# Performance work log

Hardware: AMD Instinct MI355X
Metric: run time of the kernel (lower is better)

The kernel has to match this reference:

```python
import jax, jax.numpy as jnp
import numpy as np

DEGREE = 3
N_BASIS = 16


def _clamped_knots(n_basis, degree):
    # Clamped uniform knot vector on [0, 1]: degree+1 repeated knots at each end.
    n_interior = n_basis - degree - 1
    interior = np.linspace(0.0, 1.0, n_interior + 2)[1:-1]
    knots = np.concatenate([np.zeros(degree + 1), interior, np.ones(degree + 1)])
    return jnp.asarray(knots, dtype=jnp.float32)


def bspline_basis(x, degree=DEGREE, n_basis=N_BASIS):
    # Cox-de Boor recursion, vectorized over all leading dims of x.
    # x: (...,) in [0,1] -> (..., n_basis)
    t = _clamped_knots(n_basis, degree)
    n_knots = n_basis + degree + 1
    xe = jnp.clip(x, 0.0, 1.0 - 1e-6)[..., None]
    B = ((xe >= t[:-1]) & (xe < t[1:])).astype(x.dtype)  # (..., n_knots-1)
    for p in range(1, degree + 1):
        dl = t[p:n_knots - 1] - t[:n_knots - 1 - p]
        dr = t[p + 1:n_knots] - t[1:n_knots - p]
        left = jnp.where(dl > 0, (xe - t[:n_knots - 1 - p]) / jnp.where(dl > 0, dl, 1.0), 0.0)
        right = jnp.where(dr > 0, (t[p + 1:n_knots] - xe) / jnp.where(dr > 0, dr, 1.0), 0.0)
        B = left * B[..., :-1] + right * B[..., 1:]
    return B  # (..., n_basis)


def _kl(cm, lv):
    # KL(N(cm, exp(lv)) || N(0, 1)) summed over all edges/coeffs (prior_scale = 1).
    var = jnp.exp(lv)
    return 0.5 * jnp.sum(var + cm * cm - 1.0 - lv)


def _layer(x, cm, lv):
    # x: (B, in); cm, lv: (out, in, n_basis)
    basis = bspline_basis(x)  # (B, in, n_basis)
    out = jnp.einsum('bik,oik->bo', basis, cm)  # fused per-edge weighted sum
    return out, _kl(cm, lv)


def setup_inputs() -> dict:
    key = jax.random.key(0)
    ks = jax.random.split(key, 4)
    B = 8192
    sizes = [256, 512, 512, 256]
    nb = N_BASIS
    inp = {"x": jax.random.uniform(ks[0], (B, sizes[0]), dtype=jnp.float32)}
    for i in range(3):
        inp[f"cm{i}"] = 0.1 * jax.random.normal(ks[1 + i], (sizes[i + 1], sizes[i], nb), dtype=jnp.float32)
        inp[f"lv{i}"] = -2.0 * jnp.ones((sizes[i + 1], sizes[i], nb), dtype=jnp.float32)
    return inp


def reference(x, cm0, lv0, cm1, lv1, cm2, lv2):
    out = x
    kl = jnp.zeros((), x.dtype)
    for cm, lv in ((cm0, lv0), (cm1, lv1), (cm2, lv2)):
        out, k = _layer(out, cm, lv)
        kl = kl + k
    return out, kl
```

## Files before the change

### kernel.cpp

```cpp
#include <hip/hip_runtime.h>
#include <hip/hip_bf16.h>


typedef __attribute__((ext_vector_type(8))) _Float16 f16x8;
typedef __attribute__((ext_vector_type(4))) float float4v;
typedef unsigned short ushort_t;

__device__ __forceinline__ ushort_t f2h(float f) {
  _Float16 h = (_Float16)f;
  return *(ushort_t*)&h;
}
__device__ __forceinline__ float h2f(ushort_t u) {
  return (float)*(_Float16*)&u;
}

__device__ __forceinline__ void bspline_w4(float x, int& k0, float w[4]) {
  const float XMAX = 1.0f - 1e-6f;
  float xe = fminf(fmaxf(x, 0.0f), XMAX);
  int cell = (int)(xe * 13.0f);
  cell = cell > 12 ? 12 : cell;
  k0 = cell;
  int j = cell + 3;
  const float s = 1.0f / 13.0f;
  int cjm2 = max(j - 5, 0);
  int cjm1 = max(j - 4, 0);
  int cj   = j - 3;
  int cj1  = j - 2;
  int cj2  = min(j - 1, 13);
  int cj3  = min(j, 13);
  float tjm1 = cjm1 * s, tj = cj * s;
  float tjm2 = cjm2 * s;
  float tj1 = cj1 * s, tj2 = cj2 * s, tj3 = cj3 * s;
  float left1 = xe - tj, left2 = xe - tjm1, left3 = xe - tjm2;
  float right1 = tj1 - xe, right2 = tj2 - xe, right3 = tj3 - xe;
#define INV3(d) ((d) == 1 ? 13.0f : ((d) == 2 ? 6.5f : (13.0f / 3.0f)))
  float i10 = INV3(cj1 - cj);
  float i20 = INV3(cj1 - cjm1), i21 = INV3(cj2 - cj);
  float i30 = INV3(cj1 - cjm2), i31 = INV3(cj2 - cjm1), i32 = INV3(cj3 - cj);
#undef INV3
  float temp = i10;
  float N0 = right1 * temp;
  float N1 = left1 * temp;
  temp = N0 * i20;
  N0 = right1 * temp;
  float saved = left2 * temp;
  temp = N1 * i21;
  N1 = saved + right2 * temp;
  float N2 = left1 * temp;
  temp = N0 * i30;
  N0 = right1 * temp;
  saved = left3 * temp;
  temp = N1 * i31;
  N1 = saved + right2 * temp;
  saved = left2 * temp;
  temp = N2 * i32;
  N2 = saved + right3 * temp;
  float N3 = left1 * temp;
  w[0] = N0; w[1] = N1; w[2] = N2; w[3] = N3;
}

template <bool SPLIT_A>
__global__ __launch_bounds__(256, 2) void kan_layer(
    const float* __restrict__ act, const ushort_t* __restrict__ Bsw,
    float* __restrict__ outp, int IN, int OUT) {
  const int K = IN * 16;
  const int KC = K >> 3;
  __shared__ ushort_t Ah[128 * 72];
  __shared__ ushort_t Al[SPLIT_A ? 128 * 72 : 1];

  const int tid = threadIdx.x;
  const int lane = tid & 63;
  const int wv = tid >> 6;
  const int wm = wv >> 1, wn = wv & 1;
  const int quad = lane >> 4, l15 = lane & 15;
  const int b0 = blockIdx.x * 128;
  const int n0 = blockIdx.y * 128;
  const int tbase = (n0 >> 4) + wn * 4;

  float4v acc[4][4];
#pragma unroll
  for (int a = 0; a < 4; a++)
#pragma unroll
    for (int b = 0; b < 4; b++) acc[a][b] = (float4v)0.0f;

  const int gm = tid >> 1;
  const int gip = (tid & 1) * 2;

  const int nsteps = K / 64;
  const int chunk = nsteps / gridDim.z;
  const int kbeg = blockIdx.z * chunk;
  const int kend = kbeg + chunk;
  for (int kstep = kbeg; kstep < kend; ++kstep) {
    const int i0 = kstep * 4;

    const float2 xv = *(const float2*)&act[(size_t)(b0 + gm) * IN + i0 + gip];
    f16x8 bfrag[2][4];
#pragma unroll
    for (int ks = 0; ks < 2; ++ks)
#pragma unroll
      for (int nt = 0; nt < 4; ++nt) {
        size_t eoff = (((size_t)(tbase + nt)) * KC + kstep * 8 + ks * 4) * 128
                      + lane * 8;
        bfrag[ks][nt] = *(const f16x8*)&Bsw[eoff];
      }

    int k0a, k0b; float wa[4], wb[4];
    bspline_w4(xv.x, k0a, wa);
    bspline_w4(xv.y, k0b, wb);

    __syncthreads();

    {
      uint4 z; z.x = z.y = z.z = z.w = 0u;
      ushort_t* arow_h = &Ah[gm * 72 + gip * 16];
      ((uint4*)arow_h)[0] = z; ((uint4*)arow_h)[1] = z;
      ((uint4*)arow_h)[2] = z; ((uint4*)arow_h)[3] = z;
#pragma unroll
      for (int t = 0; t < 4; ++t) {
        arow_h[k0a + t] = f2h(wa[t]);
        arow_h[16 + k0b + t] = f2h(wb[t]);
      }
      if (SPLIT_A) {
        ushort_t* arow_l = &Al[gm * 72 + gip * 16];
        ((uint4*)arow_l)[0] = z; ((uint4*)arow_l)[1] = z;
        ((uint4*)arow_l)[2] = z; ((uint4*)arow_l)[3] = z;
#pragma unroll
        for (int t = 0; t < 4; ++t) {
          arow_l[k0a + t] = f2h(wa[t] - h2f(f2h(wa[t])));
          arow_l[16 + k0b + t] = f2h(wb[t] - h2f(f2h(wb[t])));
        }
      }
    }
    __syncthreads();

#pragma unroll
    for (int ks = 0; ks < 2; ++ks) {
      f16x8 ah[4], al[4];
#pragma unroll
      for (int mt = 0; mt < 4; ++mt) {
        int off = (wm * 64 + mt * 16 + l15) * 72 + ks * 32 + quad * 8;
        ah[mt] = *(const f16x8*)&Ah[off];
        if (SPLIT_A) al[mt] = *(const f16x8*)&Al[off];
      }
#pragma unroll
      for (int mt = 0; mt < 4; ++mt)
#pragma unroll
        for (int nt = 0; nt < 4; ++nt) {
          if (SPLIT_A)
            acc[mt][nt] = __builtin_amdgcn_mfma_f32_16x16x32_f16(al[mt], bfrag[ks][nt], acc[mt][nt], 0, 0, 0);
          acc[mt][nt] = __builtin_amdgcn_mfma_f32_16x16x32_f16(ah[mt], bfrag[ks][nt], acc[mt][nt], 0, 0, 0);
        }
    }
  }

#pragma unroll
  for (int mt = 0; mt < 4; ++mt)
#pragma unroll
    for (int nt = 0; nt < 4; ++nt) {
      int col = n0 + wn * 64 + nt * 16 + l15;
#pragma unroll
      for (int r = 0; r < 4; ++r) {
        int row = b0 + wm * 64 + mt * 16 + quad * 4 + r;
        atomicAdd(&outp[(size_t)row * OUT + col], acc[mt][nt][r]);
      }
    }
}

__global__ __launch_bounds__(256) void kl_convert(
    const float* __restrict__ cm, const float* __restrict__ lv,
    ushort_t* __restrict__ bsw, int G ,
    long long ngroups, float* __restrict__ klout) {
  long long i = (long long)blockIdx.x * blockDim.x + threadIdx.x;
  const long long stride = (long long)gridDim.x * blockDim.x;
  float s = 0.0f;
  for (; i < ngroups; i += stride) {
    int o = (int)(i / G);
    int kc = (int)(i - (long long)o * G);
    const float* cp = &cm[i * 8];
    const float* lp = &lv[i * 8];
    unsigned pk[4];
#pragma unroll
    for (int t = 0; t < 4; ++t) {
      float c0 = cp[2 * t], c1 = cp[2 * t + 1];
      float l0 = lp[2 * t], l1 = lp[2 * t + 1];
      pk[t] = (unsigned)f2h(c0) | ((unsigned)f2h(c1) << 16);
      s += 0.5f * (__expf(l0) + c0 * c0 - 1.0f - l0);
      s += 0.5f * (__expf(l1) + c1 * c1 - 1.0f - l1);
    }
    uint4 v; v.x = pk[0]; v.y = pk[1]; v.z = pk[2]; v.w = pk[3];
    size_t doff = (((size_t)(o >> 4) * G + kc) * 16 + (o & 15)) * 8;
    *(uint4*)&bsw[doff] = v;
  }
#pragma unroll
  for (int off = 32; off > 0; off >>= 1) s += __shfl_down(s, off, 64);
  __shared__ float red[4];
  int wv = threadIdx.x >> 6;
  if ((threadIdx.x & 63) == 0) red[wv] = s;
  __syncthreads();
  if (threadIdx.x == 0)
    atomicAdd(klout, red[0] + red[1] + red[2] + red[3]);
}

extern "C" void kernel_launch(void* const* d_in, const int* in_sizes, int n_in,
                              void* d_out, int out_size, void* d_ws, size_t ws_size,
                              hipStream_t stream) {
  const float* x   = (const float*)d_in[0];
  const float* cm0 = (const float*)d_in[1];
  const float* lv0 = (const float*)d_in[2];
  const float* cm1 = (const float*)d_in[3];
  const float* lv1 = (const float*)d_in[4];
  const float* cm2 = (const float*)d_in[5];
  const float* lv2 = (const float*)d_in[6];

  float* out = (float*)d_out;
  float* klp = out + (size_t)8192 * 256;

  char* ws = (char*)d_ws;
  float*    act1 = (float*)(ws);
  float*    act2 = (float*)(ws + ((size_t)16 << 20));
  ushort_t* b0sw = (ushort_t*)(ws + ((size_t)32 << 20));
  ushort_t* b1sw = (ushort_t*)(ws + ((size_t)36 << 20));
  ushort_t* b2sw = (ushort_t*)(ws + ((size_t)44 << 20));

  hipMemsetAsync(ws, 0, (size_t)32 << 20, stream);
  hipMemsetAsync(d_out, 0, (size_t)out_size * sizeof(float), stream);

  kl_convert<<<2048, 256, 0, stream>>>(cm0, lv0, b0sw, 256 * 2, 512LL * 256 * 2, klp);
  kl_convert<<<2048, 256, 0, stream>>>(cm1, lv1, b1sw, 512 * 2, 512LL * 512 * 2, klp);
  kl_convert<<<2048, 256, 0, stream>>>(cm2, lv2, b2sw, 512 * 2, 256LL * 512 * 2, klp);

  kan_layer<true ><<<dim3(64, 4, 4), 256, 0, stream>>>(x,    b0sw, act1, 256, 512);
  kan_layer<false><<<dim3(64, 4, 4), 256, 0, stream>>>(act1, b1sw, act2, 512, 512);
  kan_layer<false><<<dim3(64, 2, 8), 256, 0, stream>>>(act2, b2sw, out,  512, 256);
}
```

Before: 484.3 us.

## Build B-spline A fragments in registers instead of staging through LDS

Measured after the change: 815.1 us. +68.3%, slower.

```diff
diff --git a/kernel.cpp b/kernel.cpp
--- a/kernel.cpp
+++ b/kernel.cpp
@@ -59,14 +59,54 @@
   w[0] = N0; w[1] = N1; w[2] = N2; w[3] = N3;
 }
 
+__device__ __forceinline__ f16x8 place_frag(unsigned u01, unsigned u23, int k0, int h) {
+  const int p = k0 & 1;
+  const unsigned X0 = p ? (u01 << 16) : u01;
+  const unsigned X1 = p ? ((u01 >> 16) | (u23 << 16)) : u23;
+  const unsigned X2 = p ? (u23 >> 16) : 0u;
+  const int e = (k0 >> 1) - 4 * h;
+  union { unsigned u[4]; f16x8 v; } r;
+#pragma unroll
+  for (int j = 0; j < 4; ++j) {
+    const int idx = j - e;
+    unsigned t = (idx == 1) ? X1 : X0;
+    t = (idx == 2) ? X2 : t;
+    r.u[j] = ((unsigned)idx < 3u) ? t : 0u;
+  }
+  return r.v;
+}
+
+__device__ __forceinline__ void eval_pack(float x, int& k0, unsigned& u01, unsigned& u23) {
+  float w[4];
+  bspline_w4(x, k0, w);
+  u01 = (unsigned)f2h(w[0]) | ((unsigned)f2h(w[1]) << 16);
+  u23 = (unsigned)f2h(w[2]) | ((unsigned)f2h(w[3]) << 16);
+}
+
+__device__ __forceinline__ void eval_pack_split(float x, int& k0,
+                                                unsigned& uh01, unsigned& uh23,
+                                                unsigned& ul01, unsigned& ul23) {
+  float w[4];
+  bspline_w4(x, k0, w);
+  ushort_t hh[4];
+  float rl[4];
+#pragma unroll
+  for (int t = 0; t < 4; ++t) {
+    hh[t] = f2h(w[t]);
+    rl[t] = w[t] - h2f(hh[t]);
+  }
+  uh01 = (unsigned)hh[0] | ((unsigned)hh[1] << 16);
+  uh23 = (unsigned)hh[2] | ((unsigned)hh[3] << 16);
+  ul01 = (unsigned)f2h(rl[0]) | ((unsigned)f2h(rl[1]) << 16);
+  ul23 = (unsigned)f2h(rl[2]) | ((unsigned)f2h(rl[3]) << 16);
+}
+
 template <bool SPLIT_A>
 __global__ __launch_bounds__(256, 2) void kan_layer(
     const float* __restrict__ act, const ushort_t* __restrict__ Bsw,
     float* __restrict__ outp, int IN, int OUT) {
   const int K = IN * 16;
   const int KC = K >> 3;
-  __shared__ ushort_t Ah[128 * 72];
-  __shared__ ushort_t Al[SPLIT_A ? 128 * 72 : 1];
 
   const int tid = threadIdx.x;
   const int lane = tid & 63;
@@ -76,24 +116,24 @@
   const int b0 = blockIdx.x * 128;
   const int n0 = blockIdx.y * 128;
   const int tbase = (n0 >> 4) + wn * 4;
+  const int fsel = quad >> 1;
+  const int h = quad & 1;
 
   float4v acc[4][4];
 #pragma unroll
   for (int a = 0; a < 4; a++)
 #pragma unroll
     for (int b = 0; b < 4; b++) acc[a][b] = (float4v)0.0f;
-
-  const int gm = tid >> 1;
-  const int gip = (tid & 1) * 2;
 
   const int nsteps = K / 64;
   const int chunk = nsteps / gridDim.z;
   const int kbeg = blockIdx.z * chunk;
   const int kend = kbeg + chunk;
+  const int rowb = b0 + wm * 64 + l15;
+
   for (int kstep = kbeg; kstep < kend; ++kstep) {
     const int i0 = kstep * 4;
 
-    const float2 xv = *(const float2*)&act[(size_t)(b0 + gm) * IN + i0 + gip];
     f16x8 bfrag[2][4];
 #pragma unroll
     for (int ks = 0; ks < 2; ++ks)
@@ -104,52 +144,46 @@
         bfrag[ks][nt] = *(const f16x8*)&Bsw[eoff];
       }
 
-    int k0a, k0b; float wa[4], wb[4];
-    bspline_w4(xv.x, k0a, wa);
-    bspline_w4(xv.y, k0b, wb);
-
-    __syncthreads();
-
-    {
-      uint4 z; z.x = z.y = z.z = z.w = 0u;
-      ushort_t* arow_h = &Ah[gm * 72 + gip * 16];
-      ((uint4*)arow_h)[0] = z; ((uint4*)arow_h)[1] = z;
-      ((uint4*)arow_h)[2] = z; ((uint4*)arow_h)[3] = z;
-#pragma unroll
-      for (int t = 0; t < 4; ++t) {
-        arow_h[k0a + t] = f2h(wa[t]);
-        arow_h[16 + k0b + t] = f2h(wb[t]);
+#pragma unroll
+    for (int mt = 0; mt < 4; ++mt) {
+      const int row = rowb + mt * 16;
+      const float4 xv = *(const float4*)&act[(size_t)row * IN + i0];
+      const float fa = fsel ? xv.y : xv.x;
+      const float fb = fsel ? xv.w : xv.z;
+
+      if (SPLIT_A) {
+        int k0a, k0b;
+        unsigned ah01, ah23, al01, al23, bh01, bh23, bl01, bl23;
+        eval_pack_split(fa, k0a, ah01, ah23, al01, al23);
+        eval_pack_split(fb, k0b, bh01, bh23, bl01, bl23);
+        const f16x8 a0h = place_frag(ah01, ah23, k0a, h);
+        const f16x8 a0l = place_frag(al01, al23, k0a, h);
+        const f16x8 a1h = place_frag(bh01, bh23, k0b, h);
+        const f16x8 a1l = place_frag(bl01, bl23, k0b, h);
+#pragma unroll
+        for (int nt = 0; nt < 4; ++nt) {
+          acc[mt][nt] = __builtin_amdgcn_mfma_f32_16x16x32_f16(a0l, bfrag[0][nt], acc[mt][nt], 0, 0, 0);
+          acc[mt][nt] = __builtin_amdgcn_mfma_f32_16x16x32_f16(a0h, bfrag[0][nt], acc[mt][nt], 0, 0, 0);
+        }
+#pragma unroll
+        for (int nt = 0; nt < 4; ++nt) {
+          acc[mt][nt] = __builtin_amdgcn_mfma_f32_16x16x32_f16(a1l, bfrag[1][nt], acc[mt][nt], 0, 0, 0);
+          acc[mt][nt] = __builtin_amdgcn_mfma_f32_16x16x32_f16(a1h, bfrag[1][nt], acc[mt][nt], 0, 0, 0);
+        }
+      } else {
+        int k0a, k0b;
+        unsigned a01, a23, b01, b23;
+        eval_pack(fa, k0a, a01, a23);
+        eval_pack(fb, k0b, b01, b23);
+        const f16x8 a0 = place_frag(a01, a23, k0a, h);
+        const f16x8 a1 = place_frag(b01, b23, k0b, h);
+#pragma unroll
+        for (int nt = 0; nt < 4; ++nt)
+          acc[mt][nt] = __builtin_amdgcn_mfma_f32_16x16x32_f16(a0, bfrag[0][nt], acc[mt][nt], 0, 0, 0);
+#pragma unroll
+        for (int nt = 0; nt < 4; ++nt)
+          acc[mt][nt] = __builtin_amdgcn_mfma_f32_16x16x32_f16(a1, bfrag[1][nt], acc[mt][nt], 0, 0, 0);
       }
-      if (SPLIT_A) {
-        ushort_t* arow_l = &Al[gm * 72 + gip * 16];
-        ((uint4*)arow_l)[0] = z; ((uint4*)arow_l)[1] = z;
-        ((uint4*)arow_l)[2] = z; ((uint4*)arow_l)[3] = z;
-#pragma unroll
-        for (int t = 0; t < 4; ++t) {
-          arow_l[k0a + t] = f2h(wa[t] - h2f(f2h(wa[t])));
-          arow_l[16 + k0b + t] = f2h(wb[t] - h2f(f2h(wb[t])));
-        }
-      }
-    }
-    __syncthreads();
-
-#pragma unroll
-    for (int ks = 0; ks < 2; ++ks) {
-      f16x8 ah[4], al[4];
-#pragma unroll
-      for (int mt = 0; mt < 4; ++mt) {
-        int off = (wm * 64 + mt * 16 + l15) * 72 + ks * 32 + quad * 8;
-        ah[mt] = *(const f16x8*)&Ah[off];
-        if (SPLIT_A) al[mt] = *(const f16x8*)&Al[off];
-      }
-#pragma unroll
-      for (int mt = 0; mt < 4; ++mt)
-#pragma unroll
-        for (int nt = 0; nt < 4; ++nt) {
-          if (SPLIT_A)
-            acc[mt][nt] = __builtin_amdgcn_mfma_f32_16x16x32_f16(al[mt], bfrag[ks][nt], acc[mt][nt], 0, 0, 0);
-          acc[mt][nt] = __builtin_amdgcn_mfma_f32_16x16x32_f16(ah[mt], bfrag[ks][nt], acc[mt][nt], 0, 0, 0);
-        }
     }
   }
 
```

## Double-buffer LDS basis tiles and prefetch B fragments one step ahead

Applied to the files above, without the earlier changes.

New measurement: 482.0 us. Within noise of the previous version (-0.5%).

```diff
diff --git a/kernel.cpp b/kernel.cpp
--- a/kernel.cpp
+++ b/kernel.cpp
@@ -65,8 +65,8 @@
     float* __restrict__ outp, int IN, int OUT) {
   const int K = IN * 16;
   const int KC = K >> 3;
-  __shared__ ushort_t Ah[128 * 72];
-  __shared__ ushort_t Al[SPLIT_A ? 128 * 72 : 1];
+  __shared__ ushort_t Ah[2][128 * 72];
+  __shared__ ushort_t Al[SPLIT_A ? 2 : 1][SPLIT_A ? 128 * 72 : 1];
 
   const int tid = threadIdx.x;
   const int lane = tid & 63;
@@ -85,73 +85,103 @@
 
   const int gm = tid >> 1;
   const int gip = (tid & 1) * 2;
+  const float* xrow = &act[(size_t)(b0 + gm) * IN + gip];
+
+  const ushort_t* bbase[4];
+#pragma unroll
+  for (int nt = 0; nt < 4; ++nt)
+    bbase[nt] = Bsw + (size_t)(tbase + nt) * KC * 128 + lane * 8;
 
   const int nsteps = K / 64;
   const int chunk = nsteps / gridDim.z;
   const int kbeg = blockIdx.z * chunk;
   const int kend = kbeg + chunk;
-  for (int kstep = kbeg; kstep < kend; ++kstep) {
-    const int i0 = kstep * 4;
-
-    const float2 xv = *(const float2*)&act[(size_t)(b0 + gm) * IN + i0 + gip];
-    f16x8 bfrag[2][4];
-#pragma unroll
-    for (int ks = 0; ks < 2; ++ks)
-#pragma unroll
-      for (int nt = 0; nt < 4; ++nt) {
-        size_t eoff = (((size_t)(tbase + nt)) * KC + kstep * 8 + ks * 4) * 128
-                      + lane * 8;
-        bfrag[ks][nt] = *(const f16x8*)&Bsw[eoff];
-      }
-
-    int k0a, k0b; float wa[4], wb[4];
-    bspline_w4(xv.x, k0a, wa);
-    bspline_w4(xv.y, k0b, wb);
-
-    __syncthreads();
-
-    {
-      uint4 z; z.x = z.y = z.z = z.w = 0u;
-      ushort_t* arow_h = &Ah[gm * 72 + gip * 16];
-      ((uint4*)arow_h)[0] = z; ((uint4*)arow_h)[1] = z;
-      ((uint4*)arow_h)[2] = z; ((uint4*)arow_h)[3] = z;
-#pragma unroll
-      for (int t = 0; t < 4; ++t) {
-        arow_h[k0a + t] = f2h(wa[t]);
-        arow_h[16 + k0b + t] = f2h(wb[t]);
-      }
-      if (SPLIT_A) {
-        ushort_t* arow_l = &Al[gm * 72 + gip * 16];
-        ((uint4*)arow_l)[0] = z; ((uint4*)arow_l)[1] = z;
-        ((uint4*)arow_l)[2] = z; ((uint4*)arow_l)[3] = z;
-#pragma unroll
-        for (int t = 0; t < 4; ++t) {
-          arow_l[k0a + t] = f2h(wa[t] - h2f(f2h(wa[t])));
-          arow_l[16 + k0b + t] = f2h(wb[t] - h2f(f2h(wb[t])));
-        }
-      }
-    }
-    __syncthreads();
-
-#pragma unroll
-    for (int ks = 0; ks < 2; ++ks) {
-      f16x8 ah[4], al[4];
-#pragma unroll
-      for (int mt = 0; mt < 4; ++mt) {
-        int off = (wm * 64 + mt * 16 + l15) * 72 + ks * 32 + quad * 8;
-        ah[mt] = *(const f16x8*)&Ah[off];
-        if (SPLIT_A) al[mt] = *(const f16x8*)&Al[off];
-      }
-#pragma unroll
-      for (int mt = 0; mt < 4; ++mt)
-#pragma unroll
-        for (int nt = 0; nt < 4; ++nt) {
-          if (SPLIT_A)
-            acc[mt][nt] = __builtin_amdgcn_mfma_f32_16x16x32_f16(al[mt], bfrag[ks][nt], acc[mt][nt], 0, 0, 0);
-          acc[mt][nt] = __builtin_amdgcn_mfma_f32_16x16x32_f16(ah[mt], bfrag[ks][nt], acc[mt][nt], 0, 0, 0);
-        }
-    }
-  }
+  const int klast = kend - 1;
+
+#define EVAL_WRITE(BUF, XV)                                                   \
+  {                                                                           \
+    int k0a, k0b; float wa[4], wb[4];                                         \
+    bspline_w4((XV).x, k0a, wa);                                              \
+    bspline_w4((XV).y, k0b, wb);                                              \
+    uint4 z4; z4.x = z4.y = z4.z = z4.w = 0u;                                 \
+    ushort_t* arow_h = &Ah[BUF][gm * 72 + gip * 16];                          \
+    ((uint4*)arow_h)[0] = z4; ((uint4*)arow_h)[1] = z4;                       \
+    ((uint4*)arow_h)[2] = z4; ((uint4*)arow_h)[3] = z4;                       \
+    _Pragma("unroll")                                                         \
+    for (int t = 0; t < 4; ++t) {                                             \
+      arow_h[k0a + t] = f2h(wa[t]);                                           \
+      arow_h[16 + k0b + t] = f2h(wb[t]);                                      \
+    }                                                                         \
+    if (SPLIT_A) {                                                            \
+      ushort_t* arow_l = &Al[BUF][gm * 72 + gip * 16];                        \
+      ((uint4*)arow_l)[0] = z4; ((uint4*)arow_l)[1] = z4;                     \
+      ((uint4*)arow_l)[2] = z4; ((uint4*)arow_l)[3] = z4;                     \
+      _Pragma("unroll")                                                       \
+      for (int t = 0; t < 4; ++t) {                                           \
+        arow_l[k0a + t] = f2h(wa[t] - h2f(f2h(wa[t])));                       \
+        arow_l[16 + k0b + t] = f2h(wb[t] - h2f(f2h(wb[t])));                  \
+      }                                                                       \
+    }                                                                         \
+  }
+
+#define MFMA_STEP(BUF, BF)                                                    \
+  _Pragma("unroll")                                                           \
+  for (int ks = 0; ks < 2; ++ks) {                                            \
+    f16x8 ahf[4], alf[4];                                                     \
+    _Pragma("unroll")                                                         \
+    for (int mt = 0; mt < 4; ++mt) {                                          \
+      int off = (wm * 64 + mt * 16 + l15) * 72 + ks * 32 + quad * 8;          \
+      ahf[mt] = *(const f16x8*)&Ah[BUF][off];                                 \
+      if (SPLIT_A) alf[mt] = *(const f16x8*)&Al[BUF][off];                    \
+    }                                                                         \
+    _Pragma("unroll")                                                         \
+    for (int mt = 0; mt < 4; ++mt)                                            \
+      _Pragma("unroll")                                                       \
+      for (int nt = 0; nt < 4; ++nt) {                                        \
+        if (SPLIT_A)                                                          \
+          acc[mt][nt] = __builtin_amdgcn_mfma_f32_16x16x32_f16(               \
+              alf[mt], (BF)[ks][nt], acc[mt][nt], 0, 0, 0);                   \
+        acc[mt][nt] = __builtin_amdgcn_mfma_f32_16x16x32_f16(                 \
+            ahf[mt], (BF)[ks][nt], acc[mt][nt], 0, 0, 0);                     \
+      }                                                                       \
+  }
+
+#define KSTEP_BODY(KS, CUR, BFC, BFN, XVC, XVN)                               \
+  {                                                                           \
+    const int kp1 = ((KS) + 1 <= klast) ? (KS) + 1 : klast;                   \
+    const int kp2 = ((KS) + 2 <= klast) ? (KS) + 2 : klast;                   \
+    _Pragma("unroll")                                                         \
+    for (int ks = 0; ks < 2; ++ks)                                            \
+      _Pragma("unroll")                                                       \
+      for (int nt = 0; nt < 4; ++nt)                                          \
+        BFN[ks][nt] =                                                         \
+            *(const f16x8*)&bbase[nt][(size_t)kp1 * 1024 + ks * 512];         \
+    XVN = *(const float2*)&xrow[kp2 * 4];                                     \
+    MFMA_STEP(CUR, BFC);                                                      \
+    EVAL_WRITE((CUR) ^ 1, XVC);                                               \
+    __syncthreads();                                                          \
+  }
+
+  f16x8 bf0[2][4], bf1[2][4];
+#pragma unroll
+  for (int ks = 0; ks < 2; ++ks)
+#pragma unroll
+    for (int nt = 0; nt < 4; ++nt)
+      bf0[ks][nt] = *(const f16x8*)&bbase[nt][(size_t)kbeg * 1024 + ks * 512];
+  float2 xvP = *(const float2*)&xrow[kbeg * 4];
+  float2 xv0 = *(const float2*)&xrow[((kbeg + 1 <= klast) ? kbeg + 1 : klast) * 4];
+  float2 xv1;
+  EVAL_WRITE(0, xvP);
+  __syncthreads();
+
+  for (int k = kbeg; k < kend; k += 2) {
+    KSTEP_BODY(k,     0, bf0, bf1, xv0, xv1);
+    KSTEP_BODY(k + 1, 1, bf1, bf0, xv1, xv0);
+  }
+
+#undef KSTEP_BODY
+#undef MFMA_STEP
+#undef EVAL_WRITE
 
 #pragma unroll
   for (int mt = 0; mt < 4; ++mt)
```
